# Kernel tuning notes

Measured on AMD Instinct MI355X. Metric: run time of the kernel, lower is better.

The kernel has to match this reference:

```python
import jax, jax.numpy as jnp
import numpy as np

B, L, T_BASE = 8192, 512, 4
T = T_BASE + 2            # +START, +STOP
START, STOP = T_BASE, T_BASE + 1
NEG = -10000.0


def setup_inputs() -> dict:
    key = jax.random.key(0)
    k1, k2, k3, k4 = jax.random.split(key, 4)
    feats = jax.random.normal(k1, (B, L, T), dtype=jnp.float32)
    trans = jax.random.normal(k2, (T, T), dtype=jnp.float32)
    # transitions[START, :] = -10000 (never transition out of nothing into START... i.e. into START)
    trans = trans.at[START, :].set(NEG)
    # transitions[:, STOP] = -10000 (never transition from STOP)
    trans = trans.at[:, STOP].set(NEG)
    tags = jax.random.randint(k3, (B, L), 0, T_BASE, dtype=jnp.int64)
    seq_lengths = jax.random.randint(k4, (B,), 1, L + 1, dtype=jnp.int32)
    return {"feats": feats, "transitions": trans, "tags": tags, "seq_lengths": seq_lengths}


def _crf_nll(feats, trans, tags, seq_lengths):
    # feats: [B, L, T], trans: [T, T] with trans[next, prev], tags: [B, L], seq_lengths: [B]
    mask = (jnp.arange(L)[None, :] < seq_lengths[:, None])  # [B, L] bool

    # ---- forward algorithm (log partition), batched over B, scanned over time ----
    init_alpha = jnp.full((feats.shape[0], T), NEG, dtype=feats.dtype).at[:, START].set(0.0)

    def step(alpha, xs):
        feat_t, mask_t = xs  # [B, T], [B]
        # scores[b, next, prev] = alpha[b, prev] + trans[next, prev]
        scores = alpha[:, None, :] + trans[None, :, :]
        new_alpha = jax.nn.logsumexp(scores, axis=-1) + feat_t  # [B, T]
        alpha = jnp.where(mask_t[:, None], new_alpha, alpha)
        return alpha, None

    feats_t = jnp.swapaxes(feats, 0, 1)   # [L, B, T]
    mask_t = jnp.swapaxes(mask, 0, 1)     # [L, B]
    alpha, _ = jax.lax.scan(step, init_alpha, (feats_t, mask_t))
    log_z = jax.nn.logsumexp(alpha + trans[STOP][None, :], axis=-1)  # [B]

    # ---- gold path score, fully vectorized ----
    tags32 = tags.astype(jnp.int32)
    start_col = jnp.full((tags32.shape[0], 1), START, dtype=jnp.int32)
    tags_ext = jnp.concatenate([start_col, tags32], axis=1)  # [B, L+1]
    trans_sc = trans[tags_ext[:, 1:], tags_ext[:, :-1]]       # [B, L]
    emit_sc = jnp.take_along_axis(feats, tags32[..., None], axis=2)[..., 0]  # [B, L]
    maskf = mask.astype(feats.dtype)
    gold = jnp.sum(maskf * (trans_sc + emit_sc), axis=1)      # [B]
    last_tag = jnp.take_along_axis(tags32, (seq_lengths[:, None] - 1).astype(jnp.int32), axis=1)[:, 0]
    gold = gold + trans[STOP, last_tag]

    return jnp.sum(log_z - gold) / feats.shape[0]


def reference(feats, transitions, tags, seq_lengths):
    return _crf_nll(feats, transitions, tags, seq_lengths)
```

## Files before the change

kernel.cpp:

```cpp
#include <hip/hip_runtime.h>


#define BB 8192
#define LL 512
#define LN2F 0.69314718055994530942f

__device__ __forceinline__ float uniformf(float x) {
    return __uint_as_float(__builtin_amdgcn_readfirstlane(__float_as_uint(x)));
}

#define RENORM16(P, MEX)                                                \
  do {                                                                  \
    float m_ = fmaxf(P[0], P[1]);                                       \
    _Pragma("unroll") for (int z_ = 2; z_ < 16; ++z_) m_ = fmaxf(m_, P[z_]); \
    const int ee_ = (int)((__float_as_uint(m_) >> 23) & 255) - 127;     \
    const float sc_ = __uint_as_float((unsigned)(127 - ee_) << 23);     \
    _Pragma("unroll") for (int z_ = 0; z_ < 16; ++z_) P[z_] *= sc_;     \
    MEX += ee_;                                                         \
  } while (0)

#define STEP(S, F0, F1, F2, F3, TG, PV)                                 \
  do {                                                                  \
    const bool act_ = (base + (S)) < len;                               \
    const float f0_=(F0), f1_=(F1), f2_=(F2), f3_=(F3);                 \
    const float fe0_=__expf(f0_), fe1_=__expf(f1_);                     \
    const float fe2_=__expf(f2_), fe3_=__expf(f3_);                     \
    _Pragma("unroll")                                                   \
    for (int j = 0; j < 4; ++j) {                                       \
      const float c0_=P[0*4+j], c1_=P[1*4+j], c2_=P[2*4+j], c3_=P[3*4+j]; \
      const float t0_ = fmaf(E[0], c0_, fmaf(E[1], c1_, fmaf(E[2], c2_, E[3] *c3_))); \
      const float t1_ = fmaf(E[4], c0_, fmaf(E[5], c1_, fmaf(E[6], c2_, E[7] *c3_))); \
      const float t2_ = fmaf(E[8], c0_, fmaf(E[9], c1_, fmaf(E[10],c2_, E[11]*c3_))); \
      const float t3_ = fmaf(E[12],c0_, fmaf(E[13],c1_, fmaf(E[14],c2_, E[15]*c3_))); \
      P[0*4+j] = act_ ? fe0_*t0_ : P[0*4+j];                            \
      P[1*4+j] = act_ ? fe1_*t1_ : P[1*4+j];                            \
      P[2*4+j] = act_ ? fe2_*t2_ : P[2*4+j];                            \
      P[3*4+j] = act_ ? fe3_*t3_ : P[3*4+j];                            \
    }                                                                   \
    const float lut_ = sT[(TG) * 6 + (PV)];                             \
    const float em_  = ((TG) & 2) ? (((TG) & 1) ? f3_ : f2_)            \
                                  : (((TG) & 1) ? f1_ : f0_);           \
    gold += act_ ? (lut_ + em_) : 0.f;                                  \
  } while (0)

#define TGAT(S)  ((int)((tpk >> (2*(S))) & 3u))
#define STEPE(S) STEP((S), F0[(S)/2].x, F0[(S)/2].y, F0[(S)/2].z, F0[(S)/2].w, TGAT(S), TGAT((S)-1))
#define STEPO(S) STEP((S), F1[(S)/2].x, F1[(S)/2].y, F2[(S)/2].x, F2[(S)/2].y, TGAT(S), TGAT((S)-1))

__global__ __launch_bounds__(256, 4) void crf_tree(
    const float* __restrict__ feats,
    const float* __restrict__ trans,
    const int*   __restrict__ tags,
    const int*   __restrict__ lens,
    float* __restrict__ partials)
{
    __shared__ float sT[36];

    const int tid  = threadIdx.x;
    const int lane = tid & 63;
    const int wv   = tid >> 6;
    const int g    = lane >> 5;
    const int c    = lane & 31;
    const int b    = blockIdx.x * 8 + wv * 2 + g;

    if (tid < 36) sT[tid] = trans[tid];
    __syncthreads();

    float E[16], e4[4], e5[4];
    #pragma unroll
    for (int i = 0; i < 16; ++i)
        E[i] = uniformf(__expf(sT[(i >> 2) * 6 + (i & 3)]));
    #pragma unroll
    for (int i = 0; i < 4; ++i) {
        e4[i] = uniformf(__expf(sT[i * 6 + 4]));
        e5[i] = uniformf(__expf(sT[30 + i]));
    }

    const int len = lens[b];

    const int wmax  = max(len, __shfl_xor(len, 32, 64));
    const int seg2  = __builtin_amdgcn_readfirstlane(((wmax + 31) >> 5) + 1) & ~1;
    const int npair = __builtin_amdgcn_readfirstlane(seg2 >> 1);
    const int base  = c * seg2;
    const bool seg0 = (c == 0);

    const float* fp  = feats + (size_t)b * (LL * 6) + (size_t)base * 6;
    const int*   tbp = tags  + (size_t)b * LL + base;
    const int pv0 = seg0 ? 4 : (tbp[-1] & 3);

    float4 F0[8]; float2 F1[8], F2[8];
    #pragma unroll
    for (int p = 0; p < 8; ++p)
        if (p < npair) {
            const float* q = fp + p * 12;
            F0[p] = *(const float4*)(q);
            F1[p] = *(const float2*)(q + 6);
            F2[p] = *(const float2*)(q + 8);
        }
    unsigned tpk = 0;
    #pragma unroll
    for (int q = 0; q < 4; ++q)
        if (q * 4 < seg2) {
            const int4 t = *(const int4*)(tbp + q * 4);
            tpk |= (unsigned)(t.x & 3) << (2*(q*4+0));
            tpk |= (unsigned)(t.y & 3) << (2*(q*4+1));
            tpk |= (unsigned)(t.z & 3) << (2*(q*4+2));
            tpk |= (unsigned)(t.w & 3) << (2*(q*4+3));
        }

    float P[16];
    #pragma unroll
    for (int z = 0; z < 16; ++z) P[z] = (z % 5 == 0) ? 1.f : 0.f;
    int   mex  = 0;
    float gold = 0.f;

    {
        const bool act_ = base < len;
        const float f0_=F0[0].x, f1_=F0[0].y, f2_=F0[0].z, f3_=F0[0].w;
        const float fe0_=__expf(f0_), fe1_=__expf(f1_);
        const float fe2_=__expf(f2_), fe3_=__expf(f3_);
        #pragma unroll
        for (int j = 0; j < 4; ++j) {
            const float u0 = seg0 ? e4[0] : E[0*4+j];
            const float u1 = seg0 ? e4[1] : E[1*4+j];
            const float u2 = seg0 ? e4[2] : E[2*4+j];
            const float u3 = seg0 ? e4[3] : E[3*4+j];
            P[0*4+j] = act_ ? fe0_*u0 : P[0*4+j];
            P[1*4+j] = act_ ? fe1_*u1 : P[1*4+j];
            P[2*4+j] = act_ ? fe2_*u2 : P[2*4+j];
            P[3*4+j] = act_ ? fe3_*u3 : P[3*4+j];
        }
        const int t0 = TGAT(0);
        const float lut_ = sT[t0 * 6 + pv0];
        const float em_  = (t0 & 2) ? ((t0 & 1) ? f3_ : f2_)
                                    : ((t0 & 1) ? f1_ : f0_);
        gold += act_ ? (lut_ + em_) : 0.f;
        STEPO(1);
    }
    if (npair > 1) { STEPE(2);  STEPO(3);  RENORM16(P, mex); }
    if (npair > 2) { STEPE(4);  STEPO(5);  }
    if (npair > 3) { STEPE(6);  STEPO(7);  RENORM16(P, mex); }
    if (npair > 4) { STEPE(8);  STEPO(9);  }
    if (npair > 5) { STEPE(10); STEPO(11); RENORM16(P, mex); }
    if (npair > 6) { STEPE(12); STEPO(13); }
    if (npair > 7) { STEPE(14); STEPO(15); RENORM16(P, mex); }

    {
        const unsigned dl = (unsigned)(len - 1 - base);
        if (dl < (unsigned)seg2) gold += sT[30 + (int)((tpk >> (2*dl)) & 3u)];
    }

    #pragma unroll
    for (int k = 1; k <= 8; k <<= 1) {
        float Q[16];
        #pragma unroll
        for (int z = 0; z < 16; ++z) Q[z] = __shfl_down(P[z], k, 32);
        const int mq = __shfl_down(mex, k, 32);
        float N[16];
        #pragma unroll
        for (int i = 0; i < 4; ++i)
            #pragma unroll
            for (int j = 0; j < 4; ++j)
                N[i*4+j] = fmaf(Q[i*4+0], P[0*4+j], fmaf(Q[i*4+1], P[1*4+j],
                           fmaf(Q[i*4+2], P[2*4+j], Q[i*4+3] * P[3*4+j])));
        #pragma unroll
        for (int z = 0; z < 16; ++z) P[z] = N[z];
        mex += mq;
        if (k == 2 || k == 8) RENORM16(P, mex);
    }

    float al0, al1, al2, al3;
    {
        float Q[16];
        #pragma unroll
        for (int z = 0; z < 16; ++z) Q[z] = __shfl_down(P[z], 16, 32);
        const int mq = __shfl_down(mex, 16, 32);
        al0 = fmaf(Q[0], P[0], fmaf(Q[1], P[4], fmaf(Q[2], P[8], Q[3] *P[12])));
        al1 = fmaf(Q[4], P[0], fmaf(Q[5], P[4], fmaf(Q[6], P[8], Q[7] *P[12])));
        al2 = fmaf(Q[8], P[0], fmaf(Q[9], P[4], fmaf(Q[10],P[8], Q[11]*P[12])));
        al3 = fmaf(Q[12],P[0], fmaf(Q[13],P[4], fmaf(Q[14],P[8], Q[15]*P[12])));
        mex += mq;
    }

    #pragma unroll
    for (int k = 1; k <= 16; k <<= 1)
        gold += __shfl_xor(gold, k, 32);

    const float dot = fmaf(e5[0], al0, fmaf(e5[1], al1,
                      fmaf(e5[2], al2, e5[3] * al3)));
    const float logz = fmaf((float)mex, LN2F, __logf(dot));
    if (c == 0)
        partials[b] = logz - gold;
}

__global__ __launch_bounds__(256) void k_reduce(const float* __restrict__ partials,
                                               float* __restrict__ out)
{
    __shared__ float sh[256];
    const int t = threadIdx.x;
    float s = 0.f;
    #pragma unroll
    for (int j = 0; j < 32; ++j) s += partials[t + 256 * j];
    sh[t] = s;
    __syncthreads();
    #pragma unroll
    for (int d = 128; d > 0; d >>= 1) {
        if (t < d) sh[t] += sh[t + d];
        __syncthreads();
    }
    if (t == 0) out[0] = sh[0] * (1.0f / 8192.0f);
}

extern "C" void kernel_launch(void* const* d_in, const int* in_sizes, int n_in,
                              void* d_out, int out_size, void* d_ws, size_t ws_size,
                              hipStream_t stream) {
    const float* feats = (const float*)d_in[0];
    const float* trans = (const float*)d_in[1];
    const int*   tags  = (const int*)d_in[2];
    const int*   lens  = (const int*)d_in[3];
    float* out = (float*)d_out;
    float* partials = (float*)d_ws;

    crf_tree<<<BB / 8, 256, 0, stream>>>(feats, trans, tags, lens, partials);
    k_reduce<<<1, 256, 0, stream>>>(partials, out);
}
```

Baseline: 32.18 us.

## Split feature and tag loads into two phases overlapping compute, raise occupancy

Loads only the first four feature pairs and tag quads up front, then issues the remaining loads after the first steps so their latency overlaps with computation. Moves the exp-table setup after the first loads and hoists the length load ahead of the barrier. Raises the launch-bounds occupancy hint from 4 to 6 blocks per CU, which caps registers per thread and may cause spills.

```diff
diff --git a/kernel.cpp b/kernel.cpp
--- a/kernel.cpp
+++ b/kernel.cpp
@@ -47,7 +47,15 @@
 #define STEPE(S) STEP((S), F0[(S)/2].x, F0[(S)/2].y, F0[(S)/2].z, F0[(S)/2].w, TGAT(S), TGAT((S)-1))
 #define STEPO(S) STEP((S), F1[(S)/2].x, F1[(S)/2].y, F2[(S)/2].x, F2[(S)/2].y, TGAT(S), TGAT((S)-1))
 
-__global__ __launch_bounds__(256, 4) void crf_tree(
+#define MERGET(Q, TI)                                                   \
+  do {                                                                  \
+    tpk |= (unsigned)((TI).x & 3) << (2*((Q)*4+0));                     \
+    tpk |= (unsigned)((TI).y & 3) << (2*((Q)*4+1));                     \
+    tpk |= (unsigned)((TI).z & 3) << (2*((Q)*4+2));                     \
+    tpk |= (unsigned)((TI).w & 3) << (2*((Q)*4+3));                     \
+  } while (0)
+
+__global__ __launch_bounds__(256, 6) void crf_tree(
     const float* __restrict__ feats,
     const float* __restrict__ trans,
     const int*   __restrict__ tags,
@@ -63,20 +71,9 @@
     const int c    = lane & 31;
     const int b    = blockIdx.x * 8 + wv * 2 + g;
 
+    const int len = lens[b];
     if (tid < 36) sT[tid] = trans[tid];
     __syncthreads();
-
-    float E[16], e4[4], e5[4];
-    #pragma unroll
-    for (int i = 0; i < 16; ++i)
-        E[i] = uniformf(__expf(sT[(i >> 2) * 6 + (i & 3)]));
-    #pragma unroll
-    for (int i = 0; i < 4; ++i) {
-        e4[i] = uniformf(__expf(sT[i * 6 + 4]));
-        e5[i] = uniformf(__expf(sT[30 + i]));
-    }
-
-    const int len = lens[b];
 
     const int wmax  = max(len, __shfl_xor(len, 32, 64));
     const int seg2  = __builtin_amdgcn_readfirstlane(((wmax + 31) >> 5) + 1) & ~1;
@@ -90,23 +87,30 @@
 
     float4 F0[8]; float2 F1[8], F2[8];
     #pragma unroll
-    for (int p = 0; p < 8; ++p)
+    for (int p = 0; p < 4; ++p)
         if (p < npair) {
             const float* q = fp + p * 12;
             F0[p] = *(const float4*)(q);
             F1[p] = *(const float2*)(q + 6);
             F2[p] = *(const float2*)(q + 8);
         }
+    int4 tq0, tq1;
+    tq0 = *(const int4*)tbp;
+    if (npair > 2) tq1 = *(const int4*)(tbp + 4);
+
+    float E[16], e4[4], e5[4];
+    #pragma unroll
+    for (int i = 0; i < 16; ++i)
+        E[i] = uniformf(__expf(sT[(i >> 2) * 6 + (i & 3)]));
+    #pragma unroll
+    for (int i = 0; i < 4; ++i) {
+        e4[i] = uniformf(__expf(sT[i * 6 + 4]));
+        e5[i] = uniformf(__expf(sT[30 + i]));
+    }
+
     unsigned tpk = 0;
-    #pragma unroll
-    for (int q = 0; q < 4; ++q)
-        if (q * 4 < seg2) {
-            const int4 t = *(const int4*)(tbp + q * 4);
-            tpk |= (unsigned)(t.x & 3) << (2*(q*4+0));
-            tpk |= (unsigned)(t.y & 3) << (2*(q*4+1));
-            tpk |= (unsigned)(t.z & 3) << (2*(q*4+2));
-            tpk |= (unsigned)(t.w & 3) << (2*(q*4+3));
-        }
+    MERGET(0, tq0);
+    if (npair > 2) MERGET(1, tq1);
 
     float P[16];
     #pragma unroll
@@ -135,14 +139,27 @@
         const float em_  = (t0 & 2) ? ((t0 & 1) ? f3_ : f2_)
                                     : ((t0 & 1) ? f1_ : f0_);
         gold += act_ ? (lut_ + em_) : 0.f;
-        STEPO(1);
+        STEP(1, F1[0].x, F1[0].y, F2[0].x, F2[0].y, TGAT(1), t0);
     }
     if (npair > 1) { STEPE(2);  STEPO(3);  RENORM16(P, mex); }
+
+    #pragma unroll
+    for (int p = 4; p < 8; ++p)
+        if (p < npair) {
+            const float* q = fp + p * 12;
+            F0[p] = *(const float4*)(q);
+            F1[p] = *(const float2*)(q + 6);
+            F2[p] = *(const float2*)(q + 8);
+        }
+    int4 tq2, tq3;
+    if (npair > 4) tq2 = *(const int4*)(tbp + 8);
+    if (npair > 6) tq3 = *(const int4*)(tbp + 12);
+
     if (npair > 2) { STEPE(4);  STEPO(5);  }
     if (npair > 3) { STEPE(6);  STEPO(7);  RENORM16(P, mex); }
-    if (npair > 4) { STEPE(8);  STEPO(9);  }
+    if (npair > 4) { MERGET(2, tq2); STEPE(8);  STEPO(9);  }
     if (npair > 5) { STEPE(10); STEPO(11); RENORM16(P, mex); }
-    if (npair > 6) { STEPE(12); STEPO(13); }
+    if (npair > 6) { MERGET(3, tq3); STEPE(12); STEPO(13); }
     if (npair > 7) { STEPE(14); STEPO(15); RENORM16(P, mex); }
 
     {
```

New measurement: 43.29 us. +34.5%, slower.
